# Kernel optimization log

Hardware: AMD Instinct MI355X
Metric: run time of the kernel (lower is better)

## Reference

```python
import jax, jax.numpy as jnp
from jax import lax
import numpy as np

T, B, D_IN, H = 2048, 8, 1024, 1024
DELTA_INIT = -1.8

def setup_inputs() -> dict:
    key = jax.random.key(0)
    ks = jax.random.split(key, 4)
    std = 1.0 / np.sqrt(H)
    x = jax.random.normal(ks[0], (T, B, D_IN), dtype=jnp.float32)
    h0 = jnp.zeros((B, H), dtype=jnp.float32)
    Wx = jax.random.uniform(ks[1], (H, D_IN), minval=-std, maxval=std, dtype=jnp.float32)
    R = jax.random.uniform(ks[2], (H, H), minval=-std, maxval=std, dtype=jnp.float32)
    bias = jnp.zeros((H,), dtype=jnp.float32)
    W_delta = jax.random.uniform(ks[3], (H, D_IN), minval=-std * 0.1, maxval=std * 0.1, dtype=jnp.float32)
    b_delta = jnp.full((H,), DELTA_INIT, dtype=jnp.float32)
    return {"x": x, "h0": h0, "Wx": Wx, "R": R, "bias": bias, "W_delta": W_delta, "b_delta": b_delta}

def reference(x, h0, Wx, R, bias, W_delta, b_delta):
    # Precompute input projections for all timesteps (parallel GEMMs)
    xw = jnp.einsum('tbi,hi->tbh', x, Wx) + bias           # [T,B,H]
    delta_raw = jnp.einsum('tbi,hi->tbh', x, W_delta) + b_delta  # [T,B,H]
    decay = jnp.exp(-jax.nn.softplus(delta_raw))           # in (0,1)

    def step(h, inp):
        xw_t, decay_t = inp
        cand = jnp.tanh(h @ R.T + xw_t)                    # [B,H]
        h_new = decay_t * h + (1.0 - decay_t) * cand
        return h_new, h_new

    _, hs = lax.scan(step, h0, (xw, decay))
    return hs  # [T,B,H] == h[1:] in the torch module
```

## Files before the change

kernel.cpp:

```cpp
#include <hip/hip_runtime.h>

#define TT 2048
#define BB 8
#define DD 1024
#define HH 1024
#define CHB 128

typedef unsigned int u32;
typedef unsigned short u16;
typedef unsigned long long u64;
typedef float f32x4 __attribute__((ext_vector_type(4)));
typedef u32 u32x2 __attribute__((ext_vector_type(2)));
typedef _Float16 f16x8 __attribute__((ext_vector_type(8)));

static __device__ __forceinline__ u16 f16bits(float x) {
    _Float16 h = (_Float16)x;
    u16 r;
    __builtin_memcpy(&r, &h, 2);
    return r;
}

static __device__ __forceinline__ float fast_tanh(float x) {
    const float ax = __builtin_fabsf(x);
    const float e = __builtin_amdgcn_exp2f(ax * -2.885390082f);
    const float r = (1.0f - e) * __builtin_amdgcn_rcpf(1.0f + e);
    return __builtin_copysignf(r, x);
}

__global__ __launch_bounds__(256) void clear_hb_kernel(u32* hb) {
    const int i = blockIdx.x * 256 + threadIdx.x;
    __hip_atomic_store(&hb[i], 0xFFFF0000u, __ATOMIC_RELAXED, __HIP_MEMORY_SCOPE_AGENT);
}

__global__ __launch_bounds__(256) void proj_kernel(
    const float* __restrict__ x, const float* __restrict__ Wx,
    const float* __restrict__ Wd, const float* __restrict__ bias,
    const float* __restrict__ bdel, float* __restrict__ xw_out,
    float* __restrict__ decay_out)
{
    __shared__ __align__(16) _Float16 xs[64][40];
    __shared__ __align__(16) _Float16 wxs[64][40];
    __shared__ __align__(16) _Float16 wds[64][40];

    const int tid = threadIdx.x;
    const int bm = blockIdx.y * 64;
    const int bn = blockIdx.x * 64;
    const int w = tid >> 6, l = tid & 63;
    const int ar = l & 15, kg = l >> 4;
    const int srow = tid >> 2, scol = (tid & 3) * 8;

    f32x4 accx[4], accd[4];
#pragma unroll
    for (int ct = 0; ct < 4; ++ct) {
        accx[ct] = (f32x4){0.f, 0.f, 0.f, 0.f};
        accd[ct] = (f32x4){0.f, 0.f, 0.f, 0.f};
    }

    for (int k0 = 0; k0 < DD; k0 += 32) {
        const float* xp = &x[(size_t)(bm + srow) * DD + k0 + scol];
        const float* wxp = &Wx[(size_t)(bn + srow) * DD + k0 + scol];
        const float* wdp = &Wd[(size_t)(bn + srow) * DD + k0 + scol];
        f32x4 a0 = *(const f32x4*)xp,  a1 = *(const f32x4*)(xp + 4);
        f32x4 b0 = *(const f32x4*)wxp, b1 = *(const f32x4*)(wxp + 4);
        f32x4 c0 = *(const f32x4*)wdp, c1 = *(const f32x4*)(wdp + 4);
        f16x8 ha, hb_, hc;
#pragma unroll
        for (int e = 0; e < 4; ++e) {
            ha[e] = (_Float16)a0[e];  ha[e + 4] = (_Float16)a1[e];
            hb_[e] = (_Float16)b0[e]; hb_[e + 4] = (_Float16)b1[e];
            hc[e] = (_Float16)c0[e];  hc[e + 4] = (_Float16)c1[e];
        }
        __syncthreads();
        *(f16x8*)&xs[srow][scol] = ha;
        *(f16x8*)&wxs[srow][scol] = hb_;
        *(f16x8*)&wds[srow][scol] = hc;
        __syncthreads();

        const f16x8 af = *(const f16x8*)&xs[w * 16 + ar][kg * 8];
#pragma unroll
        for (int ct = 0; ct < 4; ++ct) {
            const f16x8 bfx = *(const f16x8*)&wxs[ct * 16 + ar][kg * 8];
            const f16x8 bfd = *(const f16x8*)&wds[ct * 16 + ar][kg * 8];
            accx[ct] = __builtin_amdgcn_mfma_f32_16x16x32_f16(af, bfx, accx[ct], 0, 0, 0);
            accd[ct] = __builtin_amdgcn_mfma_f32_16x16x32_f16(af, bfd, accd[ct], 0, 0, 0);
        }
    }

#pragma unroll
    for (int ct = 0; ct < 4; ++ct) {
        const int col = bn + ct * 16 + ar;
        const float bx = bias[col];
        const float bd = bdel[col];
#pragma unroll
        for (int j = 0; j < 4; ++j) {
            const int row = bm + w * 16 + kg * 4 + j;
            xw_out[(size_t)row * HH + col] = accx[ct][j] + bx;
            decay_out[(size_t)row * HH + col] = 1.0f / (1.0f + expf(accd[ct][j] + bd));
        }
    }
}

__global__ __launch_bounds__(512) void scan_kernel(
    const float* __restrict__ h0, const float* __restrict__ R,
    const float* __restrict__ decay, float* __restrict__ out,
    u32* __restrict__ hb)
{
    __shared__ __align__(16) _Float16 hst[2][HH];

    const int tid = threadIdx.x;
    const int w = tid >> 6;
    const int l = tid & 63;
    const int ar = l & 15, kg = l >> 4;
    const int b = blockIdx.x & 7, g = blockIdx.x >> 3;

    const int chrow = g * CHB + w * 16 + ar;
    f16x8 afrag[32];
#pragma unroll
    for (int s = 0; s < 32; ++s) {
        const float* rp = &R[(size_t)chrow * HH + s * 32 + kg * 8];
        const f32x4 r0 = *(const f32x4*)rp;
        const f32x4 r1 = *(const f32x4*)(rp + 4);
        f16x8 a;
#pragma unroll
        for (int e = 0; e < 4; ++e) { a[e] = (_Float16)r0[e]; a[e + 4] = (_Float16)r1[e]; }
        afrag[s] = a;
    }

    const bool pollme = ((tid >> 6) != g);

    const bool ep = (ar < 4);
    const int ch = g * CHB + w * 16 + kg * 4 + ar;
    const int chloc = w * 16 + kg * 4 + ar;
    float hp = 0.f, xw_c = 0.f, d_c = 0.f;
    if (ep) {
        hp = h0[(size_t)b * HH + ch];
        xw_c = out[(size_t)b * HH + ch];
        d_c = decay[(size_t)b * HH + ch];
    }

    for (int t = 0; t < TT; ++t) {
        const int p = t & 1;
        if (t == 0) {
            const float2 v = *(const float2*)&h0[(size_t)b * HH + tid * 2];
            *(u32*)&hst[0][tid * 2] = (u32)f16bits(v.x) | ((u32)f16bits(v.y) << 16);
        } else if (pollme) {
            const u32 expt = (u32)(t - 1) << 16;
            const u64 gp = (u64)hb
                         + (u64)(((t - 1) & 1) * (BB * HH) + b * HH + tid * 2) * 4;
            u32x2 gA, gB, gr;
            asm volatile("global_load_dwordx2 %0, %1, off sc0 sc1"
                         : "=v"(gA) : "v"(gp));
            __builtin_amdgcn_s_sleep(4);
            asm volatile("global_load_dwordx2 %0, %1, off sc0 sc1"
                         : "=v"(gB) : "v"(gp));
            while (true) {
                asm volatile("s_waitcnt vmcnt(1)" ::: "memory");
                __builtin_amdgcn_sched_barrier(0);
                if (!(((gA[0] ^ expt) | (gA[1] ^ expt)) & 0xffff0000u)) { gr = gA; break; }
                asm volatile("global_load_dwordx2 %0, %1, off sc0 sc1"
                             : "=v"(gA) : "v"(gp));
                asm volatile("s_waitcnt vmcnt(1)" ::: "memory");
                __builtin_amdgcn_sched_barrier(0);
                if (!(((gB[0] ^ expt) | (gB[1] ^ expt)) & 0xffff0000u)) { gr = gB; break; }
                asm volatile("global_load_dwordx2 %0, %1, off sc0 sc1"
                             : "=v"(gB) : "v"(gp));
            }
            asm volatile("s_waitcnt vmcnt(0)" ::: "memory");
            __builtin_amdgcn_sched_barrier(0);
            *(u32*)&hst[p][tid * 2] = (gr[0] & 0xffffu) | (gr[1] << 16);
        }
        __syncthreads();

        float xw_n = xw_c, d_n = d_c;
        if (ep && t + 1 < TT) {
            const size_t nidx = (size_t)(t + 1) * (BB * HH) + (size_t)b * HH + ch;
            xw_n = out[nidx];
            d_n = decay[nidx];
        }

        f32x4 ac0 = {0.f, 0.f, 0.f, 0.f}, ac1 = ac0, ac2 = ac0, ac3 = ac0;
#pragma unroll
        for (int s = 0; s < 32; s += 4) {
            ac0 = __builtin_amdgcn_mfma_f32_16x16x32_f16(
                      afrag[s + 0], *(const f16x8*)&hst[p][(s + 0) * 32 + kg * 8], ac0, 0, 0, 0);
            ac1 = __builtin_amdgcn_mfma_f32_16x16x32_f16(
                      afrag[s + 1], *(const f16x8*)&hst[p][(s + 1) * 32 + kg * 8], ac1, 0, 0, 0);
            ac2 = __builtin_amdgcn_mfma_f32_16x16x32_f16(
                      afrag[s + 2], *(const f16x8*)&hst[p][(s + 2) * 32 + kg * 8], ac2, 0, 0, 0);
            ac3 = __builtin_amdgcn_mfma_f32_16x16x32_f16(
                      afrag[s + 3], *(const f16x8*)&hst[p][(s + 3) * 32 + kg * 8], ac3, 0, 0, 0);
        }
        const f32x4 acc = (ac0 + ac1) + (ac2 + ac3);

        if (ep) {
            const float s = (ar == 0) ? acc[0] : (ar == 1) ? acc[1]
                          : (ar == 2) ? acc[2] : acc[3];
            const float cand = fast_tanh(s + xw_c);
            const float hnew = d_c * hp + (1.0f - d_c) * cand;
            hp = hnew;
            const u16 hbits = f16bits(hnew);
            const u32 gran = ((u32)t << 16) | (u32)hbits;
            const u64 dst = (u64)hb + (u64)((t & 1) * (BB * HH) + b * HH + ch) * 4;
            asm volatile("global_store_dword %0, %1, off sc0 sc1"
                         :: "v"(dst), "v"(gran) : "memory");
            hst[p ^ 1][g * CHB + chloc] = *(const _Float16*)&hbits;
            out[(size_t)t * (BB * HH) + (size_t)b * HH + ch] = hnew;
        }
        xw_c = xw_n;
        d_c = d_n;
    }
}

extern "C" void kernel_launch(void* const* d_in, const int* in_sizes, int n_in,
                              void* d_out, int out_size, void* d_ws, size_t ws_size,
                              hipStream_t stream) {
    const float* x    = (const float*)d_in[0];
    const float* h0   = (const float*)d_in[1];
    const float* Wx   = (const float*)d_in[2];
    const float* R    = (const float*)d_in[3];
    const float* bias = (const float*)d_in[4];
    const float* Wd   = (const float*)d_in[5];
    const float* bdel = (const float*)d_in[6];
    float* out = (float*)d_out;

    float* decay = (float*)d_ws;
    u32* hb = (u32*)((char*)d_ws + (size_t)TT * BB * HH * 4);

    clear_hb_kernel<<<64, 256, 0, stream>>>(hb);
    proj_kernel<<<dim3(HH / 64, (TT * BB) / 64), 256, 0, stream>>>(
        x, Wx, Wd, bias, bdel, out, decay);
    scan_kernel<<<64, 512, 0, stream>>>(h0, R, decay, out, hb);
}
```

Before: 3.274 ms.

## Split recurrent matvec along K across waves with LDS reduction

Each wave now covers a 128-wide K slice for all 8 output tiles of the block, instead of the full K range for a single 16-row tile. There are 8 independent MFMA accumulator chains per wave rather than 4 dependent-chain accumulators, and each wave reads only 4 B fragments from LDS. Partial sums go to an LDS buffer, and the first 128 threads reduce them after an extra barrier before the elementwise update. This shortens the serial MFMA dependency chain on the per-step critical path, at the cost of an additional __syncthreads and LDS traffic each timestep.

```diff
diff --git a/kernel.cpp b/kernel.cpp
--- a/kernel.cpp
+++ b/kernel.cpp
@@ -106,6 +106,7 @@
     u32* __restrict__ hb)
 {
     __shared__ __align__(16) _Float16 hst[2][HH];
+    __shared__ __align__(16) float red[8][136];
 
     const int tid = threadIdx.x;
     const int w = tid >> 6;
@@ -113,29 +114,29 @@
     const int ar = l & 15, kg = l >> 4;
     const int b = blockIdx.x & 7, g = blockIdx.x >> 3;
 
-    const int chrow = g * CHB + w * 16 + ar;
-    f16x8 afrag[32];
-#pragma unroll
-    for (int s = 0; s < 32; ++s) {
-        const float* rp = &R[(size_t)chrow * HH + s * 32 + kg * 8];
-        const f32x4 r0 = *(const f32x4*)rp;
-        const f32x4 r1 = *(const f32x4*)(rp + 4);
-        f16x8 a;
-#pragma unroll
-        for (int e = 0; e < 4; ++e) { a[e] = (_Float16)r0[e]; a[e + 4] = (_Float16)r1[e]; }
-        afrag[s] = a;
-    }
+    f16x8 afrag[8][4];
+#pragma unroll
+    for (int c = 0; c < 8; ++c)
+#pragma unroll
+        for (int s = 0; s < 4; ++s) {
+            const float* rp = &R[(size_t)(g * CHB + c * 16 + ar) * HH
+                                 + w * 128 + s * 32 + kg * 8];
+            const f32x4 r0 = *(const f32x4*)rp;
+            const f32x4 r1 = *(const f32x4*)(rp + 4);
+            f16x8 a;
+#pragma unroll
+            for (int e = 0; e < 4; ++e) { a[e] = (_Float16)r0[e]; a[e + 4] = (_Float16)r1[e]; }
+            afrag[c][s] = a;
+        }
 
     const bool pollme = ((tid >> 6) != g);
 
-    const bool ep = (ar < 4);
-    const int ch = g * CHB + w * 16 + kg * 4 + ar;
-    const int chloc = w * 16 + kg * 4 + ar;
+    const bool ep = (tid < CHB);
     float hp = 0.f, xw_c = 0.f, d_c = 0.f;
     if (ep) {
-        hp = h0[(size_t)b * HH + ch];
-        xw_c = out[(size_t)b * HH + ch];
-        d_c = decay[(size_t)b * HH + ch];
+        hp = h0[(size_t)b * HH + g * CHB + tid];
+        xw_c = out[(size_t)b * HH + g * CHB + tid];
+        d_c = decay[(size_t)b * HH + g * CHB + tid];
     }
 
     for (int t = 0; t < TT; ++t) {
@@ -173,38 +174,46 @@
 
         float xw_n = xw_c, d_n = d_c;
         if (ep && t + 1 < TT) {
-            const size_t nidx = (size_t)(t + 1) * (BB * HH) + (size_t)b * HH + ch;
+            const size_t nidx = (size_t)(t + 1) * (BB * HH) + (size_t)b * HH + g * CHB + tid;
             xw_n = out[nidx];
             d_n = decay[nidx];
         }
 
-        f32x4 ac0 = {0.f, 0.f, 0.f, 0.f}, ac1 = ac0, ac2 = ac0, ac3 = ac0;
-#pragma unroll
-        for (int s = 0; s < 32; s += 4) {
-            ac0 = __builtin_amdgcn_mfma_f32_16x16x32_f16(
-                      afrag[s + 0], *(const f16x8*)&hst[p][(s + 0) * 32 + kg * 8], ac0, 0, 0, 0);
-            ac1 = __builtin_amdgcn_mfma_f32_16x16x32_f16(
-                      afrag[s + 1], *(const f16x8*)&hst[p][(s + 1) * 32 + kg * 8], ac1, 0, 0, 0);
-            ac2 = __builtin_amdgcn_mfma_f32_16x16x32_f16(
-                      afrag[s + 2], *(const f16x8*)&hst[p][(s + 2) * 32 + kg * 8], ac2, 0, 0, 0);
-            ac3 = __builtin_amdgcn_mfma_f32_16x16x32_f16(
-                      afrag[s + 3], *(const f16x8*)&hst[p][(s + 3) * 32 + kg * 8], ac3, 0, 0, 0);
-        }
-        const f32x4 acc = (ac0 + ac1) + (ac2 + ac3);
+        f16x8 bf[4];
+#pragma unroll
+        for (int s = 0; s < 4; ++s)
+            bf[s] = *(const f16x8*)&hst[p][w * 128 + s * 32 + kg * 8];
+        f32x4 acc[8];
+#pragma unroll
+        for (int c = 0; c < 8; ++c) acc[c] = (f32x4){0.f, 0.f, 0.f, 0.f};
+#pragma unroll
+        for (int s = 0; s < 4; ++s)
+#pragma unroll
+            for (int c = 0; c < 8; ++c)
+                acc[c] = __builtin_amdgcn_mfma_f32_16x16x32_f16(
+                             afrag[c][s], bf[s], acc[c], 0, 0, 0);
+
+        if (ar == 0) {
+#pragma unroll
+            for (int c = 0; c < 8; ++c)
+                *(f32x4*)&red[w][c * 16 + kg * 4] = acc[c];
+        }
+        __syncthreads();
 
         if (ep) {
-            const float s = (ar == 0) ? acc[0] : (ar == 1) ? acc[1]
-                          : (ar == 2) ? acc[2] : acc[3];
+            float s = red[0][tid] + red[1][tid] + red[2][tid] + red[3][tid]
+                    + red[4][tid] + red[5][tid] + red[6][tid] + red[7][tid];
             const float cand = fast_tanh(s + xw_c);
             const float hnew = d_c * hp + (1.0f - d_c) * cand;
             hp = hnew;
             const u16 hbits = f16bits(hnew);
             const u32 gran = ((u32)t << 16) | (u32)hbits;
-            const u64 dst = (u64)hb + (u64)((t & 1) * (BB * HH) + b * HH + ch) * 4;
+            const u64 dst = (u64)hb
+                          + (u64)((t & 1) * (BB * HH) + b * HH + g * CHB + tid) * 4;
             asm volatile("global_store_dword %0, %1, off sc0 sc1"
                          :: "v"(dst), "v"(gran) : "memory");
-            hst[p ^ 1][g * CHB + chloc] = *(const _Float16*)&hbits;
-            out[(size_t)t * (BB * HH) + (size_t)b * HH + ch] = hnew;
+            hst[p ^ 1][g * CHB + tid] = *(const _Float16*)&hbits;
+            out[(size_t)t * (BB * HH) + (size_t)b * HH + g * CHB + tid] = hnew;
         }
         xw_c = xw_n;
         d_c = d_n;
```

After: 3.805 ms. +16.2%, slower.

## Repartition scan by hidden rows with split-K across waves and per-block sentinels

Applied to the files above, without the earlier changes.

The recurrent scan now gives each of 64 blocks 16 hidden rows for all 8 batches. The K dimension is split across 8 waves, whose partial MFMA sums are reduced through shared memory. Blocks publish f16 hidden state plus a per-block step counter sentinel, replacing tagged per-element flags. Each wave then loads its h slice straight from global memory instead of staging the full state in LDS. This cuts per-block R fragment registers and the redundant MFMA work of the batch-per-block layout, at the cost of an extra barrier, reduction traffic, and polling 64 sentinels plus a dependent global load every step.

```diff
diff --git a/kernel.cpp b/kernel.cpp
--- a/kernel.cpp
+++ b/kernel.cpp
@@ -4,20 +4,19 @@
 #define BB 8
 #define DD 1024
 #define HH 1024
-#define CHB 128
+#define NBLK 64
 
 typedef unsigned int u32;
 typedef unsigned short u16;
 typedef unsigned long long u64;
 typedef float f32x4 __attribute__((ext_vector_type(4)));
-typedef u32 u32x2 __attribute__((ext_vector_type(2)));
 typedef _Float16 f16x8 __attribute__((ext_vector_type(8)));
 
-static __device__ __forceinline__ u16 f16bits(float x) {
+static __device__ __forceinline__ u32 f16bits(float x) {
     _Float16 h = (_Float16)x;
     u16 r;
     __builtin_memcpy(&r, &h, 2);
-    return r;
+    return (u32)r;
 }
 
 static __device__ __forceinline__ float fast_tanh(float x) {
@@ -27,9 +26,8 @@
     return __builtin_copysignf(r, x);
 }
 
-__global__ __launch_bounds__(256) void clear_hb_kernel(u32* hb) {
-    const int i = blockIdx.x * 256 + threadIdx.x;
-    __hip_atomic_store(&hb[i], 0xFFFF0000u, __ATOMIC_RELAXED, __HIP_MEMORY_SCOPE_AGENT);
+__global__ __launch_bounds__(64) void clear_sent_kernel(u32* sent) {
+    __hip_atomic_store(&sent[threadIdx.x], 0u, __ATOMIC_RELAXED, __HIP_MEMORY_SCOPE_AGENT);
 }
 
 __global__ __launch_bounds__(256) void proj_kernel(
@@ -92,10 +90,10 @@
         const float bx = bias[col];
         const float bd = bdel[col];
 #pragma unroll
-        for (int j = 0; j < 4; ++j) {
-            const int row = bm + w * 16 + kg * 4 + j;
-            xw_out[(size_t)row * HH + col] = accx[ct][j] + bx;
-            decay_out[(size_t)row * HH + col] = 1.0f / (1.0f + expf(accd[ct][j] + bd));
+        for (int jj = 0; jj < 4; ++jj) {
+            const int row = bm + w * 16 + kg * 4 + jj;
+            xw_out[(size_t)row * HH + col] = accx[ct][jj] + bx;
+            decay_out[(size_t)row * HH + col] = 1.0f / (1.0f + expf(accd[ct][jj] + bd));
         }
     }
 }
@@ -103,21 +101,20 @@
 __global__ __launch_bounds__(512) void scan_kernel(
     const float* __restrict__ h0, const float* __restrict__ R,
     const float* __restrict__ decay, float* __restrict__ out,
-    u32* __restrict__ hb)
+    u16* __restrict__ hdata, u32* __restrict__ sent)
 {
-    __shared__ __align__(16) _Float16 hst[2][HH];
+    __shared__ float red[8][8][20];
 
     const int tid = threadIdx.x;
-    const int w = tid >> 6;
-    const int l = tid & 63;
+    const int w = tid >> 6, l = tid & 63;
     const int ar = l & 15, kg = l >> 4;
-    const int b = blockIdx.x & 7, g = blockIdx.x >> 3;
-
-    const int chrow = g * CHB + w * 16 + ar;
-    f16x8 afrag[32];
-#pragma unroll
-    for (int s = 0; s < 32; ++s) {
-        const float* rp = &R[(size_t)chrow * HH + s * 32 + kg * 8];
+    const int j = blockIdx.x;
+    const int bcol = l & 7;
+
+    f16x8 afrag[4];
+#pragma unroll
+    for (int s = 0; s < 4; ++s) {
+        const float* rp = &R[(size_t)(j * 16 + ar) * HH + w * 128 + s * 32 + kg * 8];
         const f32x4 r0 = *(const f32x4*)rp;
         const f32x4 r1 = *(const f32x4*)(rp + 4);
         f16x8 a;
@@ -126,88 +123,112 @@
         afrag[s] = a;
     }
 
-    const bool pollme = ((tid >> 6) != g);
-
-    const bool ep = (ar < 4);
-    const int ch = g * CHB + w * 16 + kg * 4 + ar;
-    const int chloc = w * 16 + kg * 4 + ar;
-    float hp = 0.f, xw_c = 0.f, d_c = 0.f;
-    if (ep) {
-        hp = h0[(size_t)b * HH + ch];
-        xw_c = out[(size_t)b * HH + ch];
-        d_c = decay[(size_t)b * HH + ch];
+    const int eb = l >> 3, ec = (l & 7) * 2;
+    const int gch = j * 16 + ec;
+    float hp0 = 0.f, hp1 = 0.f, xw0 = 0.f, xw1 = 0.f, dc0 = 0.f, dc1 = 0.f;
+    if (w == 7) {
+        hp0 = h0[(size_t)eb * HH + gch];
+        hp1 = h0[(size_t)eb * HH + gch + 1];
+        const float2 xv = *(const float2*)&out[(size_t)eb * HH + gch];
+        const float2 dv = *(const float2*)&decay[(size_t)eb * HH + gch];
+        xw0 = xv.x; xw1 = xv.y; dc0 = dv.x; dc1 = dv.y;
     }
 
     for (int t = 0; t < TT; ++t) {
-        const int p = t & 1;
-        if (t == 0) {
-            const float2 v = *(const float2*)&h0[(size_t)b * HH + tid * 2];
-            *(u32*)&hst[0][tid * 2] = (u32)f16bits(v.x) | ((u32)f16bits(v.y) << 16);
-        } else if (pollme) {
-            const u32 expt = (u32)(t - 1) << 16;
-            const u64 gp = (u64)hb
-                         + (u64)(((t - 1) & 1) * (BB * HH) + b * HH + tid * 2) * 4;
-            u32x2 gA, gB, gr;
-            asm volatile("global_load_dwordx2 %0, %1, off sc0 sc1"
-                         : "=v"(gA) : "v"(gp));
+        if (t > 0 && w == 0) {
+            const u64 sp = (u64)(sent + l);
+            const u32 tv = (u32)t;
+            u32 sA, sB;
+            asm volatile("global_load_dword %0, %1, off sc0 sc1" : "=v"(sA) : "v"(sp));
             __builtin_amdgcn_s_sleep(4);
-            asm volatile("global_load_dwordx2 %0, %1, off sc0 sc1"
-                         : "=v"(gB) : "v"(gp));
+            asm volatile("global_load_dword %0, %1, off sc0 sc1" : "=v"(sB) : "v"(sp));
             while (true) {
                 asm volatile("s_waitcnt vmcnt(1)" ::: "memory");
                 __builtin_amdgcn_sched_barrier(0);
-                if (!(((gA[0] ^ expt) | (gA[1] ^ expt)) & 0xffff0000u)) { gr = gA; break; }
-                asm volatile("global_load_dwordx2 %0, %1, off sc0 sc1"
-                             : "=v"(gA) : "v"(gp));
+                if (sA >= tv) break;
+                asm volatile("global_load_dword %0, %1, off sc0 sc1" : "=v"(sA) : "v"(sp));
                 asm volatile("s_waitcnt vmcnt(1)" ::: "memory");
                 __builtin_amdgcn_sched_barrier(0);
-                if (!(((gB[0] ^ expt) | (gB[1] ^ expt)) & 0xffff0000u)) { gr = gB; break; }
-                asm volatile("global_load_dwordx2 %0, %1, off sc0 sc1"
-                             : "=v"(gB) : "v"(gp));
+                if (sB >= tv) break;
+                asm volatile("global_load_dword %0, %1, off sc0 sc1" : "=v"(sB) : "v"(sp));
             }
             asm volatile("s_waitcnt vmcnt(0)" ::: "memory");
             __builtin_amdgcn_sched_barrier(0);
-            *(u32*)&hst[p][tid * 2] = (gr[0] & 0xffffu) | (gr[1] << 16);
-        }
-        __syncthreads();
-
-        float xw_n = xw_c, d_n = d_c;
-        if (ep && t + 1 < TT) {
-            const size_t nidx = (size_t)(t + 1) * (BB * HH) + (size_t)b * HH + ch;
-            xw_n = out[nidx];
-            d_n = decay[nidx];
-        }
-
-        f32x4 ac0 = {0.f, 0.f, 0.f, 0.f}, ac1 = ac0, ac2 = ac0, ac3 = ac0;
-#pragma unroll
-        for (int s = 0; s < 32; s += 4) {
-            ac0 = __builtin_amdgcn_mfma_f32_16x16x32_f16(
-                      afrag[s + 0], *(const f16x8*)&hst[p][(s + 0) * 32 + kg * 8], ac0, 0, 0, 0);
-            ac1 = __builtin_amdgcn_mfma_f32_16x16x32_f16(
-                      afrag[s + 1], *(const f16x8*)&hst[p][(s + 1) * 32 + kg * 8], ac1, 0, 0, 0);
-            ac2 = __builtin_amdgcn_mfma_f32_16x16x32_f16(
-                      afrag[s + 2], *(const f16x8*)&hst[p][(s + 2) * 32 + kg * 8], ac2, 0, 0, 0);
-            ac3 = __builtin_amdgcn_mfma_f32_16x16x32_f16(
-                      afrag[s + 3], *(const f16x8*)&hst[p][(s + 3) * 32 + kg * 8], ac3, 0, 0, 0);
-        }
-        const f32x4 acc = (ac0 + ac1) + (ac2 + ac3);
-
-        if (ep) {
-            const float s = (ar == 0) ? acc[0] : (ar == 1) ? acc[1]
-                          : (ar == 2) ? acc[2] : acc[3];
-            const float cand = fast_tanh(s + xw_c);
-            const float hnew = d_c * hp + (1.0f - d_c) * cand;
-            hp = hnew;
-            const u16 hbits = f16bits(hnew);
-            const u32 gran = ((u32)t << 16) | (u32)hbits;
-            const u64 dst = (u64)hb + (u64)((t & 1) * (BB * HH) + b * HH + ch) * 4;
+        }
+        __syncthreads();
+
+        float xn0 = xw0, xn1 = xw1, dn0 = dc0, dn1 = dc1;
+        if (w == 7 && t + 1 < TT) {
+            const size_t nx = (size_t)(t + 1) * (BB * HH) + (size_t)eb * HH + gch;
+            const float2 xv = *(const float2*)&out[nx];
+            const float2 dv = *(const float2*)&decay[nx];
+            xn0 = xv.x; xn1 = xv.y; dn0 = dv.x; dn1 = dv.y;
+        }
+
+        f16x8 bf0, bf1, bf2, bf3;
+        if (t == 0) {
+            f16x8 tmp[4];
+#pragma unroll
+            for (int s = 0; s < 4; ++s) {
+                const float* hq = &h0[(size_t)bcol * HH + w * 128 + s * 32 + kg * 8];
+                const f32x4 v0 = *(const f32x4*)hq;
+                const f32x4 v1 = *(const f32x4*)(hq + 4);
+                f16x8 b;
+#pragma unroll
+                for (int e = 0; e < 4; ++e) { b[e] = (_Float16)v0[e]; b[e + 4] = (_Float16)v1[e]; }
+                tmp[s] = b;
+            }
+            bf0 = tmp[0]; bf1 = tmp[1]; bf2 = tmp[2]; bf3 = tmp[3];
+        } else {
+            const u64 hb = (u64)hdata
+                         + (u64)(((t - 1) & 1) * (BB * HH) + bcol * HH + w * 128 + kg * 8) * 2;
+            asm volatile(
+                "global_load_dwordx4 %0, %4, off sc0 sc1\n\t"
+                "global_load_dwordx4 %1, %4, off offset:64 sc0 sc1\n\t"
+                "global_load_dwordx4 %2, %4, off offset:128 sc0 sc1\n\t"
+                "global_load_dwordx4 %3, %4, off offset:192 sc0 sc1\n\t"
+                "s_waitcnt vmcnt(0)"
+                : "=&v"(bf0), "=&v"(bf1), "=&v"(bf2), "=&v"(bf3)
+                : "v"(hb) : "memory");
+            __builtin_amdgcn_sched_barrier(0);
+        }
+
+        f32x4 acc = {0.f, 0.f, 0.f, 0.f};
+        acc = __builtin_amdgcn_mfma_f32_16x16x32_f16(afrag[0], bf0, acc, 0, 0, 0);
+        acc = __builtin_amdgcn_mfma_f32_16x16x32_f16(afrag[1], bf1, acc, 0, 0, 0);
+        acc = __builtin_amdgcn_mfma_f32_16x16x32_f16(afrag[2], bf2, acc, 0, 0, 0);
+        acc = __builtin_amdgcn_mfma_f32_16x16x32_f16(afrag[3], bf3, acc, 0, 0, 0);
+
+        if (ar < 8) *(f32x4*)&red[w][ar][kg * 4] = acc;
+        __syncthreads();
+
+        if (w == 7) {
+            float s0 = 0.f, s1 = 0.f;
+#pragma unroll
+            for (int ww = 0; ww < 8; ++ww) {
+                const float2 rv = *(const float2*)&red[ww][eb][ec];
+                s0 += rv.x; s1 += rv.y;
+            }
+            const float c0 = fast_tanh(s0 + xw0);
+            const float c1 = fast_tanh(s1 + xw1);
+            const float h0n = dc0 * hp0 + (1.0f - dc0) * c0;
+            const float h1n = dc1 * hp1 + (1.0f - dc1) * c1;
+            hp0 = h0n; hp1 = h1n;
+            const u32 pk = f16bits(h0n) | (f16bits(h1n) << 16);
+            const u64 dst = (u64)hdata + (u64)((t & 1) * (BB * HH) + eb * HH + gch) * 2;
             asm volatile("global_store_dword %0, %1, off sc0 sc1"
-                         :: "v"(dst), "v"(gran) : "memory");
-            hst[p ^ 1][g * CHB + chloc] = *(const _Float16*)&hbits;
-            out[(size_t)t * (BB * HH) + (size_t)b * HH + ch] = hnew;
-        }
-        xw_c = xw_n;
-        d_c = d_n;
+                         :: "v"(dst), "v"(pk) : "memory");
+            *(float2*)&out[(size_t)t * (BB * HH) + (size_t)eb * HH + gch] =
+                make_float2(h0n, h1n);
+            asm volatile("s_waitcnt vmcnt(0)" ::: "memory");
+            if (l == 0) {
+                const u64 sp = (u64)(sent + j);
+                const u32 tv = (u32)(t + 1);
+                asm volatile("global_store_dword %0, %1, off sc0 sc1"
+                             :: "v"(sp), "v"(tv) : "memory");
+            }
+        }
+        xw0 = xn0; xw1 = xn1; dc0 = dn0; dc1 = dn1;
     }
 }
 
@@ -224,10 +245,11 @@
     float* out = (float*)d_out;
 
     float* decay = (float*)d_ws;
-    u32* hb = (u32*)((char*)d_ws + (size_t)TT * BB * HH * 4);
-
-    clear_hb_kernel<<<64, 256, 0, stream>>>(hb);
+    u16* hdata = (u16*)((char*)d_ws + (size_t)TT * BB * HH * 4);
+    u32* sent = (u32*)((char*)hdata + 2 * BB * HH * 2);
+
+    clear_sent_kernel<<<1, 64, 0, stream>>>(sent);
     proj_kernel<<<dim3(HH / 64, (TT * BB) / 64), 256, 0, stream>>>(
         x, Wx, Wd, bias, bdel, out, decay);
-    scan_kernel<<<64, 512, 0, stream>>>(h0, R, decay, out, hb);
-}
+    scan_kernel<<<NBLK, 512, 0, stream>>>(h0, R, decay, out, hdata, sent);
+}
```

Result: slower. 9.397 ms (+187.0%).
